# Performance work log

Hardware: AMD Instinct MI355X
Metric: run time of the kernel (lower is better)

The kernel has to match this reference:

```python
import jax, jax.numpy as jnp
import numpy as np

N_BITS = 4
SIZE_SCALE = 8 // N_BITS  # 2 int4 values per byte
MASK = (1 << N_BITS) - 1  # 0xF

OC, IC = 8192, 8192
B = 64


def setup_inputs() -> dict:
    key = jax.random.key(0)
    k_in, k_w, k_d, k_z, k_b = jax.random.split(key, 5)
    input = jax.random.normal(k_in, (B, IC), dtype=jnp.float32)
    # packed uint8 weight buffer: [OC // SIZE_SCALE, IC]; stored as int32 with byte values
    weight_packed = jax.random.randint(k_w, (OC // SIZE_SCALE, IC), 0, 256, dtype=jnp.int32)
    # per-output-channel affine quant params
    delta = jax.random.uniform(k_d, (OC,), dtype=jnp.float32) * 0.01 + 1e-4
    zero_point = jax.random.uniform(k_z, (OC,), dtype=jnp.float32) * MASK
    bias = jax.random.normal(k_b, (OC,), dtype=jnp.float32)
    return {"input": input, "weight_packed": weight_packed, "delta": delta,
            "zero_point": zero_point, "bias": bias}


def _dequantize(weight_packed, delta, zero_point):
    # Bit-unpack: each byte holds SIZE_SCALE values of N_BITS each, packed along
    # the output-channel dim (dim 0), low nibble first.
    parts = [ (weight_packed >> (N_BITS * i)) & MASK for i in range(SIZE_SCALE) ]
    w_int = jnp.concatenate(parts, axis=0)               # [OC, IC] int
    # Affine dequant, per output channel: w = (q - zp) * delta
    w = (w_int.astype(jnp.float32) - zero_point[:, None]) * delta[:, None]
    return w


def reference(input, weight_packed, delta, zero_point, bias):
    # use_weight_quant=True, use_act_quant=False (defaults in the module)
    w = _dequantize(weight_packed, delta, zero_point)    # [OC, IC]
    out = jnp.dot(input, w.T) + bias                     # F.linear
    return out
```

## Files before the change

### kernel.cpp

```cpp
#include <hip/hip_runtime.h>

constexpr int BATCH = 64;
constexpr int IC    = 8192;
constexpr int OC    = 8192;
constexpr int OCH   = 4096;
constexpr int KSPLIT = 8;
constexpr int KPER  = IC / KSPLIT;
constexpr int BK    = 64;
constexpr int NITER = KPER / BK;
constexpr int LDK   = BK + 8;

typedef __bf16 bf16x8 __attribute__((ext_vector_type(8)));
typedef float  f32x4  __attribute__((ext_vector_type(4)));

static __device__ __forceinline__ unsigned short f2bf(float f) {
    unsigned u = __float_as_uint(f);
    u += 0x7FFFu + ((u >> 16) & 1u);
    return (unsigned short)(u >> 16);
}

static __device__ __forceinline__ unsigned pack2bf(int n0, int n1) {
    unsigned f0 = __float_as_uint((float)n0);
    unsigned f1 = __float_as_uint((float)n1);
    return __builtin_amdgcn_perm(f1, f0, 0x07060302u);
}

__global__ __launch_bounds__(256) void prep_kernel(
    const float* __restrict__ in, unsigned short* __restrict__ Abf,
    float* __restrict__ S)
{
    const int b = blockIdx.x;
    const int t = threadIdx.x;
    const float* row = in + (size_t)b * IC;
    unsigned short* orow = Abf + (size_t)b * IC;

    float sum = 0.f;
#pragma unroll
    for (int i = 0; i < IC / 1024; ++i) {
        const int c = i * 1024 + t * 4;
        const float4 v = *(const float4*)(row + c);
        sum += (v.x + v.y) + (v.z + v.w);
        ushort4 o = make_ushort4(f2bf(v.x), f2bf(v.y), f2bf(v.z), f2bf(v.w));
        *(ushort4*)(orow + c) = o;
    }
#pragma unroll
    for (int off = 32; off > 0; off >>= 1) sum += __shfl_down(sum, off);

    __shared__ float red[4];
    if ((t & 63) == 0) red[t >> 6] = sum;
    __syncthreads();
    if (t == 0) S[b] = (red[0] + red[1]) + (red[2] + red[3]);
}

__global__ __launch_bounds__(256, 4) void gemm_kernel(
    const unsigned short* __restrict__ Abf,
    const int* __restrict__ wp,
    float* __restrict__ part)
{
    __shared__ unsigned short lA[64 * LDK];
    __shared__ unsigned short lW[64 * LDK];

    const int t    = threadIdx.x;
    const int wave = t >> 6;
    const int lane = t & 63;
    const int lm   = lane & 15;
    const int lq   = lane >> 4;

    const int nt  = blockIdx.x & 127;
    const int ks  = blockIdx.x >> 7;
    const int r0  = nt * 32;
    const int kb0 = ks * KPER;

    f32x4 acc[4];
    const f32x4 zero4 = {0.f, 0.f, 0.f, 0.f};
#pragma unroll
    for (int i = 0; i < 4; ++i) acc[i] = zero4;

    const int uAr = t >> 2, uAc = (t & 3) * 16;
    const int uWr = t >> 3, uWc = (t & 7) * 8;

    const unsigned short* pA = Abf + (size_t)uAr * IC + kb0 + uAc;
    const int*            pW = wp  + (size_t)(r0 + uWr) * IC + kb0 + uWc;

    int4 a0 = *(const int4*)(pA);
    int4 a1 = *(const int4*)(pA + 8);
    int4 w0 = *(const int4*)(pW);
    int4 w1 = *(const int4*)(pW + 4);

    for (int it = 0; it < NITER; ++it) {
        __syncthreads();

        *(int4*)(&lA[uAr * LDK + uAc])     = a0;
        *(int4*)(&lA[uAr * LDK + uAc + 8]) = a1;

        int4 lo, hi;
        lo.x = pack2bf(w0.x & 15, w0.y & 15);
        lo.y = pack2bf(w0.z & 15, w0.w & 15);
        lo.z = pack2bf(w1.x & 15, w1.y & 15);
        lo.w = pack2bf(w1.z & 15, w1.w & 15);
        hi.x = pack2bf(w0.x >> 4, w0.y >> 4);
        hi.y = pack2bf(w0.z >> 4, w0.w >> 4);
        hi.z = pack2bf(w1.x >> 4, w1.y >> 4);
        hi.w = pack2bf(w1.z >> 4, w1.w >> 4);
        *(int4*)(&lW[uWr        * LDK + uWc]) = lo;
        *(int4*)(&lW[(uWr + 32) * LDK + uWc]) = hi;

        __syncthreads();

        {
            const int koff = ((it + 1) & (NITER - 1)) * BK;
            a0 = *(const int4*)(pA + koff);
            a1 = *(const int4*)(pA + koff + 8);
            w0 = *(const int4*)(pW + koff);
            w1 = *(const int4*)(pW + koff + 4);
        }

#pragma unroll
        for (int s = 0; s < 2; ++s) {
            const int kc = s * 32 + lq * 8;
            const bf16x8 bfrg = *(const bf16x8*)(&lW[(wave * 16 + lm) * LDK + kc]);
#pragma unroll
            for (int mt = 0; mt < 4; ++mt) {
                const bf16x8 afrg = *(const bf16x8*)(&lA[(mt * 16 + lm) * LDK + kc]);
                acc[mt] = __builtin_amdgcn_mfma_f32_16x16x32_bf16(afrg, bfrg, acc[mt], 0, 0, 0);
            }
        }
    }

    const int cr = wave * 16 + lm;
    const int ch = (cr < 32) ? (r0 + cr) : (OCH + r0 + (cr - 32));
    float* pout = part + (size_t)ks * (BATCH * OC) + ch;

#pragma unroll
    for (int mt = 0; mt < 4; ++mt) {
#pragma unroll
        for (int r = 0; r < 4; ++r) {
            const int m = mt * 16 + lq * 4 + r;
            pout[(size_t)m * OC] = acc[mt][r];
        }
    }
}

__global__ __launch_bounds__(256) void reduce_kernel(
    const float* __restrict__ part,
    const float* __restrict__ delta,
    const float* __restrict__ zp,
    const float* __restrict__ bias,
    const float* __restrict__ S,
    float* __restrict__ out)
{
    const int e  = (blockIdx.x * 256 + threadIdx.x) * 4;
    const int m  = e >> 13;
    const int ch = e & (OC - 1);

    float4 s = {0.f, 0.f, 0.f, 0.f};
#pragma unroll
    for (int k = 0; k < KSPLIT; ++k) {
        const float4 p = *(const float4*)(part + (size_t)k * (BATCH * OC) + e);
        s.x += p.x; s.y += p.y; s.z += p.z; s.w += p.w;
    }
    const float4 d = *(const float4*)(delta + ch);
    const float4 z = *(const float4*)(zp + ch);
    const float4 b = *(const float4*)(bias + ch);
    const float Sm = S[m];

    float4 o;
    o.x = d.x * s.x + b.x - d.x * z.x * Sm;
    o.y = d.y * s.y + b.y - d.y * z.y * Sm;
    o.z = d.z * s.z + b.z - d.z * z.z * Sm;
    o.w = d.w * s.w + b.w - d.w * z.w * Sm;
    *(float4*)(out + e) = o;
}

extern "C" void kernel_launch(void* const* d_in, const int* in_sizes, int n_in,
                              void* d_out, int out_size, void* d_ws, size_t ws_size,
                              hipStream_t stream) {
    const float* input = (const float*)d_in[0];
    const int*   wpk   = (const int*)d_in[1];
    const float* delta = (const float*)d_in[2];
    const float* zp    = (const float*)d_in[3];
    const float* bias  = (const float*)d_in[4];
    float* out = (float*)d_out;

    unsigned short* Abf = (unsigned short*)d_ws;
    float* S    = (float*)((char*)d_ws + (size_t)BATCH * IC * 2);
    float* part = (float*)((char*)d_ws + (size_t)BATCH * IC * 2 + 4096);

    prep_kernel<<<dim3(BATCH), dim3(256), 0, stream>>>(input, Abf, S);
    gemm_kernel<<<dim3(128 * KSPLIT), dim3(256), 0, stream>>>(Abf, wpk, part);
    reduce_kernel<<<dim3(BATCH * OC / 1024), dim3(256), 0, stream>>>(part, delta, zp, bias, S, out);
}
```

Before: 225.4 us.

## Double-buffer LDS tiles in GEMM and halve the K-split factor

Converts the GEMM main loop to ping-pong shared-memory buffers. The next tile's global loads are issued before the MFMAs on the current buffer, and dequantized/stored into the other buffer afterwards, so each iteration needs one barrier instead of two. KSPLIT drops from 8 to 4, which halves the partial-sum traffic and the reduce work but also halves the grid to 512 blocks, and launch bounds relax to 2 blocks per CU. The doubled LDS footprint and fewer blocks may reduce latency hiding for what is a memory-bound weight stream.

Measured after the change: 218.7 us. -2.9%, faster.

```diff
diff --git a/kernel.cpp b/kernel.cpp
--- a/kernel.cpp
+++ b/kernel.cpp
@@ -4,7 +4,7 @@
 constexpr int IC    = 8192;
 constexpr int OC    = 8192;
 constexpr int OCH   = 4096;
-constexpr int KSPLIT = 8;
+constexpr int KSPLIT = 4;
 constexpr int KPER  = IC / KSPLIT;
 constexpr int BK    = 64;
 constexpr int NITER = KPER / BK;
@@ -52,13 +52,13 @@
     if (t == 0) S[b] = (red[0] + red[1]) + (red[2] + red[3]);
 }
 
-__global__ __launch_bounds__(256, 4) void gemm_kernel(
+__global__ __launch_bounds__(256, 2) void gemm_kernel(
     const unsigned short* __restrict__ Abf,
     const int* __restrict__ wp,
     float* __restrict__ part)
 {
-    __shared__ unsigned short lA[64 * LDK];
-    __shared__ unsigned short lW[64 * LDK];
+    __shared__ unsigned short lA[2][64 * LDK];
+    __shared__ unsigned short lW[2][64 * LDK];
 
     const int t    = threadIdx.x;
     const int wave = t >> 6;
@@ -87,12 +87,9 @@
     int4 w0 = *(const int4*)(pW);
     int4 w1 = *(const int4*)(pW + 4);
 
-    for (int it = 0; it < NITER; ++it) {
-        __syncthreads();
-
-        *(int4*)(&lA[uAr * LDK + uAc])     = a0;
-        *(int4*)(&lA[uAr * LDK + uAc + 8]) = a1;
-
+    {
+        *(int4*)(&lA[0][uAr * LDK + uAc])     = a0;
+        *(int4*)(&lA[0][uAr * LDK + uAc + 8]) = a1;
         int4 lo, hi;
         lo.x = pack2bf(w0.x & 15, w0.y & 15);
         lo.y = pack2bf(w0.z & 15, w0.w & 15);
@@ -102,29 +99,46 @@
         hi.y = pack2bf(w0.z >> 4, w0.w >> 4);
         hi.z = pack2bf(w1.x >> 4, w1.y >> 4);
         hi.w = pack2bf(w1.z >> 4, w1.w >> 4);
-        *(int4*)(&lW[uWr        * LDK + uWc]) = lo;
-        *(int4*)(&lW[(uWr + 32) * LDK + uWc]) = hi;
-
-        __syncthreads();
-
-        {
-            const int koff = ((it + 1) & (NITER - 1)) * BK;
-            a0 = *(const int4*)(pA + koff);
-            a1 = *(const int4*)(pA + koff + 8);
-            w0 = *(const int4*)(pW + koff);
-            w1 = *(const int4*)(pW + koff + 4);
-        }
+        *(int4*)(&lW[0][uWr        * LDK + uWc]) = lo;
+        *(int4*)(&lW[0][(uWr + 32) * LDK + uWc]) = hi;
+    }
+    __syncthreads();
+
+    for (int it = 0; it < NITER; ++it) {
+        const int p = it & 1;
+
+        const int koff = ((it + 1) & (NITER - 1)) * BK;
+        a0 = *(const int4*)(pA + koff);
+        a1 = *(const int4*)(pA + koff + 8);
+        w0 = *(const int4*)(pW + koff);
+        w1 = *(const int4*)(pW + koff + 4);
 
 #pragma unroll
         for (int s = 0; s < 2; ++s) {
             const int kc = s * 32 + lq * 8;
-            const bf16x8 bfrg = *(const bf16x8*)(&lW[(wave * 16 + lm) * LDK + kc]);
+            const bf16x8 bfrg = *(const bf16x8*)(&lW[p][(wave * 16 + lm) * LDK + kc]);
 #pragma unroll
             for (int mt = 0; mt < 4; ++mt) {
-                const bf16x8 afrg = *(const bf16x8*)(&lA[(mt * 16 + lm) * LDK + kc]);
+                const bf16x8 afrg = *(const bf16x8*)(&lA[p][(mt * 16 + lm) * LDK + kc]);
                 acc[mt] = __builtin_amdgcn_mfma_f32_16x16x32_bf16(afrg, bfrg, acc[mt], 0, 0, 0);
             }
         }
+
+        *(int4*)(&lA[1 - p][uAr * LDK + uAc])     = a0;
+        *(int4*)(&lA[1 - p][uAr * LDK + uAc + 8]) = a1;
+        int4 lo, hi;
+        lo.x = pack2bf(w0.x & 15, w0.y & 15);
+        lo.y = pack2bf(w0.z & 15, w0.w & 15);
+        lo.z = pack2bf(w1.x & 15, w1.y & 15);
+        lo.w = pack2bf(w1.z & 15, w1.w & 15);
+        hi.x = pack2bf(w0.x >> 4, w0.y >> 4);
+        hi.y = pack2bf(w0.z >> 4, w0.w >> 4);
+        hi.z = pack2bf(w1.x >> 4, w1.y >> 4);
+        hi.w = pack2bf(w1.z >> 4, w1.w >> 4);
+        *(int4*)(&lW[1 - p][uWr        * LDK + uWc]) = lo;
+        *(int4*)(&lW[1 - p][(uWr + 32) * LDK + uWc]) = hi;
+
+        __syncthreads();
     }
 
     const int cr = wave * 16 + lm;
```
